# Kernel tuning notes

Hardware: AMD Instinct MI355X
Metric: run time of the kernel (lower is better)

## Reference

```python
import jax, jax.numpy as jnp
import numpy as np

D_MODEL = 768
N_HEADS = 12
D_FF = 3072
EPS = 1e-5


def _layernorm(x, g, b):
    mu = jnp.mean(x, axis=-1, keepdims=True)
    var = jnp.mean(jnp.square(x - mu), axis=-1, keepdims=True)
    return (x - mu) * jax.lax.rsqrt(var + EPS) * g + b


def setup_inputs() -> dict:
    key = jax.random.key(0)
    ks = jax.random.split(key, 16)
    d, f = D_MODEL, D_FF
    s = 1.0 / np.sqrt(d)
    inp = {
        "x": jax.random.normal(ks[0], (1, 4096, d), dtype=jnp.float32),
        "Wq": jax.random.normal(ks[1], (d, d), dtype=jnp.float32) * s,
        "bq": jnp.zeros((d,), jnp.float32),
        "Wk": jax.random.normal(ks[2], (d, d), dtype=jnp.float32) * s,
        "bk": jnp.zeros((d,), jnp.float32),
        "Wv": jax.random.normal(ks[3], (d, d), dtype=jnp.float32) * s,
        "bv": jnp.zeros((d,), jnp.float32),
        "Wo": jax.random.normal(ks[4], (d, d), dtype=jnp.float32) * s,
        "bo": jnp.zeros((d,), jnp.float32),
        "ln1_g": jnp.ones((d,), jnp.float32),
        "ln1_b": jnp.zeros((d,), jnp.float32),
        "ln2_g": jnp.ones((d,), jnp.float32),
        "ln2_b": jnp.zeros((d,), jnp.float32),
        "W1": jax.random.normal(ks[5], (d, f), dtype=jnp.float32) * s,
        "b1": jnp.zeros((f,), jnp.float32),
        "W2": jax.random.normal(ks[6], (f, d), dtype=jnp.float32) * (1.0 / np.sqrt(f)),
        "b2": jnp.zeros((d,), jnp.float32),
    }
    return inp


def reference(x, Wq, bq, Wk, bk, Wv, bv, Wo, bo, ln1_g, ln1_b, ln2_g, ln2_b, W1, b1, W2, b2):
    b, s, d = x.shape
    h = N_HEADS
    dk = d // h

    # --- attention sublayer (pre-norm residual) ---
    xn = _layernorm(x, ln1_g, ln1_b)

    def proj(W, bias):
        y = xn @ W + bias                      # [b, s, d]
        return y.reshape(b, s, h, dk).transpose(0, 2, 1, 3)  # [b, h, s, dk]

    q, k, v = proj(Wq, bq), proj(Wk, bk), proj(Wv, bv)
    scores = jnp.einsum("bhqd,bhkd->bhqk", q, k) / np.sqrt(dk)
    attn = jax.nn.softmax(scores, axis=-1)
    ctx = jnp.einsum("bhqk,bhkd->bhqd", attn, v)
    ctx = ctx.transpose(0, 2, 1, 3).reshape(b, s, d)
    x = x + (ctx @ Wo + bo)

    # --- FFN sublayer (pre-norm residual) ---
    xn2 = _layernorm(x, ln2_g, ln2_b)
    ff = jax.nn.gelu(xn2 @ W1 + b1, approximate=False) @ W2 + b2
    return x + ff
```

## Files before the change

kernel.cpp:

```cpp
#include <hip/hip_runtime.h>
#include <hip/hip_bf16.h>

typedef __attribute__((ext_vector_type(8))) __bf16 bf16x8;
typedef __attribute__((ext_vector_type(4))) __bf16 bf16x4;
typedef __attribute__((ext_vector_type(4))) float f32x4;
typedef __attribute__((ext_vector_type(4))) unsigned short u16x4;
typedef unsigned short ushort_t;

__device__ __forceinline__ ushort_t f2bf(float f) {
    union { float f; unsigned u; } v; v.f = f;
    unsigned r = v.u + 0x7fffu + ((v.u >> 16) & 1u);
    return (ushort_t)(r >> 16);
}

__device__ __forceinline__ void gload16(const ushort_t* g, ushort_t* l) {
    __builtin_amdgcn_global_load_lds(
        (const __attribute__((address_space(1))) unsigned int*)g,
        (__attribute__((address_space(3))) unsigned int*)l,
        16, 0, 0);
}

__device__ __forceinline__ void ln_row(const float* __restrict__ xr,
                                       const float* __restrict__ g,
                                       const float* __restrict__ b,
                                       ushort_t* __restrict__ orow, int t) {
    float v0 = xr[t], v1 = xr[t + 256], v2 = xr[t + 512];
    float s  = v0 + v1 + v2;
    float s2 = v0 * v0 + v1 * v1 + v2 * v2;
#pragma unroll
    for (int off = 32; off; off >>= 1) {
        s  += __shfl_down(s, off);
        s2 += __shfl_down(s2, off);
    }
    __shared__ float red[8];
    const int wid = t >> 6, lane = t & 63;
    if (lane == 0) { red[wid] = s; red[4 + wid] = s2; }
    __syncthreads();
    __shared__ float stats[2];
    if (t == 0) {
        float S = red[0] + red[1] + red[2] + red[3];
        float S2 = red[4] + red[5] + red[6] + red[7];
        float mu = S * (1.0f / 768.0f);
        float var = S2 * (1.0f / 768.0f) - mu * mu;
        stats[0] = mu;
        stats[1] = rsqrtf(var + 1e-5f);
    }
    __syncthreads();
    const float mu = stats[0], rs = stats[1];
    orow[t]       = f2bf((v0 - mu) * rs * g[t]       + b[t]);
    orow[t + 256] = f2bf((v1 - mu) * rs * g[t + 256] + b[t + 256]);
    orow[t + 512] = f2bf((v2 - mu) * rs * g[t + 512] + b[t + 512]);
}

__global__ __launch_bounds__(256) void ln_kernel(const float* __restrict__ x,
                                                 const float* __restrict__ g,
                                                 const float* __restrict__ b,
                                                 ushort_t* __restrict__ out) {
    const int row = blockIdx.x;
    ln_row(x + (size_t)row * 768, g, b, out + (size_t)row * 768, threadIdx.x);
}

__global__ __launch_bounds__(256) void prep_ln(
    const float* __restrict__ Wq, const float* __restrict__ Wk,
    const float* __restrict__ Wv, const float* __restrict__ Wo,
    const float* __restrict__ W1, const float* __restrict__ W2,
    const float* __restrict__ bq, const float* __restrict__ bk,
    const float* __restrict__ bv,
    const float* __restrict__ x, const float* __restrict__ ln1_g,
    const float* __restrict__ ln1_b,
    ushort_t* __restrict__ WqkvT, ushort_t* __restrict__ WoT,
    ushort_t* __restrict__ W1T, ushort_t* __restrict__ W2T,
    float* __restrict__ bqkv, ushort_t* __restrict__ xn) {
    const int bid = blockIdx.x;
    const int t = threadIdx.x;
    if (bid >= 6915) {
        const int row = bid - 6915;
        ln_row(x + (size_t)row * 768, ln1_g, ln1_b, xn + (size_t)row * 768, t);
        return;
    }
    if (bid >= 6912) {
        const int i = bid - 6912;
        const float* s = (i == 0) ? bq : (i == 1) ? bk : bv;
#pragma unroll
        for (int j = t; j < 768; j += 256) bqkv[i * 768 + j] = s[j];
        return;
    }
    const float* src; ushort_t* dst; int R, C, ti;
    if (bid < 576)       { src = Wq; dst = WqkvT;               R = 768;  C = 768;  ti = bid; }
    else if (bid < 1152) { src = Wk; dst = WqkvT + 768 * 768;   R = 768;  C = 768;  ti = bid - 576; }
    else if (bid < 1728) { src = Wv; dst = WqkvT + 2 * 768 * 768; R = 768; C = 768; ti = bid - 1152; }
    else if (bid < 2304) { src = Wo; dst = WoT;                 R = 768;  C = 768;  ti = bid - 1728; }
    else if (bid < 4608) { src = W1; dst = W1T;                 R = 768;  C = 3072; ti = bid - 2304; }
    else                 { src = W2; dst = W2T;                 R = 3072; C = 768;  ti = bid - 4608; }
    const int tpr = C >> 5;
    const int c0 = (ti % tpr) * 32, r0 = (ti / tpr) * 32;
    __shared__ float tile[32][33];
    {
        const int c = t & 31, r = t >> 5;
#pragma unroll
        for (int i = 0; i < 4; i++)
            tile[r + i * 8][c] = src[(size_t)(r0 + r + i * 8) * C + c0 + c];
    }
    __syncthreads();
    {
        const int oc = t >> 3, q = t & 7;
        u16x4 o;
#pragma unroll
        for (int k = 0; k < 4; k++) o[k] = f2bf(tile[q * 4 + k][oc]);
        *(u16x4*)&dst[(size_t)(c0 + oc) * R + r0 + q * 4] = o;
    }
}

template <int BN, int GELU, int RES, int OUTF, int OUTB, int OUTV>
__global__ __launch_bounds__(256, 3)
void gemm_bt(const ushort_t* __restrict__ A, const ushort_t* __restrict__ Bt,
             const float* __restrict__ bias, const float* __restrict__ res,
             float* __restrict__ outF, ushort_t* __restrict__ outB, int ldo,
             ushort_t* __restrict__ outV,
             int M, int N, int K) {
    constexpr int TR  = 128 + BN;
    constexpr int LL  = TR / 64;
    constexpr int WCF = BN / 32;
    __shared__ __align__(16) ushort_t Ls[2][TR * 32];

    const int nbx = gridDim.x;
    const int nwg = nbx * gridDim.y;
    int fb = blockIdx.y * nbx + blockIdx.x;
    fb = (fb & 7) * (nwg >> 3) + (fb >> 3);
    const int m0 = (fb / nbx) * 128, n0 = (fb % nbx) * BN;

    const int t = threadIdx.x;
    const int wid = t >> 6, lane = t & 63;
    const int wr = wid >> 1, wc = wid & 1;
    const int row16 = lane & 15, kg = lane >> 4;
    const int kb = kg * 8;

    const int srow = lane >> 2, scol = (lane & 3) * 8;
    const ushort_t* gsrc[LL];
    int lofs[LL];
#pragma unroll
    for (int i = 0; i < LL; i++) {
        const int r0 = wid * (TR / 4) + 16 * i;
        gsrc[i] = (r0 < 128 ? A + (size_t)(m0 + r0 + srow) * K
                            : Bt + (size_t)(n0 + r0 - 128 + srow) * K) + scol;
        lofs[i] = r0 * 32;
    }

#define STAGE(buf, kofs) do {                                        \
        _Pragma("unroll")                                            \
        for (int i = 0; i < LL; i++)                                 \
            gload16(gsrc[i] + (kofs), &Ls[buf][lofs[i]]);            \
    } while (0)

    f32x4 acc[4][WCF] = {};
    const int NS = K >> 5;
    STAGE(0, 0);
    STAGE(1, 32);
    int cur = 0;

    for (int s = 0; s < NS; ++s) {
        if (s + 1 == NS) asm volatile("s_waitcnt vmcnt(0)" ::: "memory");
        else             asm volatile("s_waitcnt vmcnt(%0)" :: "i"(LL) : "memory");
        __builtin_amdgcn_s_barrier();

        bf16x8 a[4], b[WCF];
#pragma unroll
        for (int i = 0; i < 4; i++)
            a[i] = *(const bf16x8*)&Ls[cur][(wr * 64 + i * 16 + row16) * 32 + kb];
#pragma unroll
        for (int j = 0; j < WCF; j++)
            b[j] = *(const bf16x8*)&Ls[cur][(128 + wc * (BN / 2) + j * 16 + row16) * 32 + kb];
        asm volatile("s_waitcnt lgkmcnt(0)" ::: "memory");
        __builtin_amdgcn_s_barrier();
        if (s + 2 < NS) STAGE(cur, (s + 2) * 32);

        __builtin_amdgcn_s_setprio(1);
#pragma unroll
        for (int i = 0; i < 4; i++)
#pragma unroll
            for (int j = 0; j < WCF; j++)
                acc[i][j] = __builtin_amdgcn_mfma_f32_16x16x32_bf16(a[i], b[j], acc[i][j], 0, 0, 0);
        __builtin_amdgcn_s_setprio(0);
        cur ^= 1;
    }
#undef STAGE

#pragma unroll
    for (int i = 0; i < 4; i++)
#pragma unroll
        for (int j = 0; j < WCF; j++) {
            const int col = n0 + wc * (BN / 2) + j * 16 + row16;
            const float bv = bias[col];
            const int rb = m0 + wr * 64 + i * 16 + kg * 4;
            if (OUTV && col >= 1536) {
                bf16x4 pk;
#pragma unroll
                for (int r = 0; r < 4; r++) pk[r] = (__bf16)(acc[i][j][r] + bv);
                *(bf16x4*)&outV[(size_t)(col - 1536) * 4096 + rb] = pk;
            } else {
#pragma unroll
                for (int r = 0; r < 4; r++) {
                    const int row = rb + r;
                    float v = acc[i][j][r] + bv;
                    if (GELU) {
                        float u = v + 0.044715f * v * v * v;
                        float e = __builtin_amdgcn_exp2f(2.30220779f * u);
                        v = v * e * __builtin_amdgcn_rcpf(e + 1.0f);
                    }
                    if (RES) v += res[(size_t)row * N + col];
                    if (OUTF) outF[(size_t)row * N + col] = v;
                    if (OUTB) outB[(size_t)row * ldo + col] = f2bf(v);
                }
            }
        }
}

__device__ __forceinline__ int swz(int row, int col) {
    return row * 64 + (col ^ ((row & 7) << 3));
}

__global__ __launch_bounds__(256, 3)
void attn_kernel(const ushort_t* __restrict__ qk,
                 const ushort_t* __restrict__ Vt,
                 float* __restrict__ num0, float* __restrict__ num1,
                 float* __restrict__ den) {
    int fb = blockIdx.y * 32 + blockIdx.x;
    fb = (fb & 7) * 96 + (fb >> 3);
    const int q0 = (fb & 31) * 128;
    const int hs = fb >> 5;
    const int h = hs >> 1, sp = hs & 1;
    const int kt0 = sp * 32;

    const int t  = threadIdx.x;
    const int w = t >> 6, lane = t & 63;
    const int row16 = lane & 15, kg = lane >> 4;
    const int kb = kg * 8;

    __shared__ __align__(16) ushort_t Ps[128 * 64];
    __shared__ __align__(16) ushort_t Ks[2][64 * 64];
    __shared__ __align__(16) ushort_t Vs[2][64 * 64];

    {
        const int qr = t >> 1, cb = (t & 1) * 32;
        const size_t qbase = (size_t)(q0 + qr) * 1536 + h * 64 + cb;
#pragma unroll
        for (int j = 0; j < 4; j++)
            *(uint4*)&Ps[swz(qr, cb + j * 8)] = *(const uint4*)&qk[qbase + j * 8];
    }
    {
        const int sr = t >> 2, sc = (t & 3) * 8;
        const size_t kbase = (size_t)(kt0 * 64 + sr) * 1536 + 768 + h * 64 + sc;
        *(uint4*)&Ks[0][swz(sr, sc)]      = *(const uint4*)&qk[kbase];
        *(uint4*)&Ks[0][swz(sr, sc + 32)] = *(const uint4*)&qk[kbase + 32];
        const size_t vbase = (size_t)(h * 64 + sr) * 4096 + kt0 * 64 + sc;
        *(uint4*)&Vs[0][swz(sr, sc)]      = *(const uint4*)&Vt[vbase];
        *(uint4*)&Vs[0][swz(sr, sc + 32)] = *(const uint4*)&Vt[vbase + 32];
    }
    bf16x8 qa0[2], qa1[2];
#pragma unroll
    for (int qb = 0; qb < 2; qb++) {
        qa0[qb] = *(const bf16x8*)&Ps[swz(w * 32 + qb * 16 + row16, kb)];
        qa1[qb] = *(const bf16x8*)&Ps[swz(w * 32 + qb * 16 + row16, 32 + kb)];
    }
    __syncthreads();

    const int rr = lane >> 3;
    const int gcol = ((lane & 7) ^ rr) * 8;
    const ushort_t* gK = qk + 768 + h * 64 + gcol + (size_t)(w * 16 + rr) * 1536;
    const ushort_t* gV = Vt + (size_t)(h * 64 + w * 16 + rr) * 4096 + gcol;

    bf16x8 vones;
#pragma unroll
    for (int i = 0; i < 8; i++) vones[i] = (__bf16)1.0f;

    f32x4 o_acc[2][4] = {};
    f32x4 o_l[2] = {};
    int cur = 0;
    const float SC = 0.18033688011112042f;

    for (int it = 0; it < 32; ++it) {
        if (it != 31) {
            const int kv1 = (kt0 + it + 1) * 64;
            ushort_t* kd = &Ks[cur ^ 1][w * 1024];
            ushort_t* vd = &Vs[cur ^ 1][w * 1024];
            gload16(gK + (size_t)kv1 * 1536,       kd);
            gload16(gK + (size_t)(kv1 + 8) * 1536, kd + 512);
            gload16(gV + kv1,                      vd);
            gload16(gV + kv1 + 8 * 4096,           vd + 512);
        }

        const ushort_t* Kc = Ks[cur];
        const ushort_t* Vc = Vs[cur];

        bf16x8 ka0[4], ka1[4];
#pragma unroll
        for (int f = 0; f < 4; f++) {
            ka0[f] = *(const bf16x8*)&Kc[swz(f * 16 + row16, kb)];
            ka1[f] = *(const bf16x8*)&Kc[swz(f * 16 + row16, 32 + kb)];
        }

        f32x4 s_acc[2][4];
        __builtin_amdgcn_s_setprio(1);
#pragma unroll
        for (int qb = 0; qb < 2; qb++)
#pragma unroll
            for (int f = 0; f < 4; f++) {
                f32x4 z = {};
                z = __builtin_amdgcn_mfma_f32_16x16x32_bf16(ka0[f], qa0[qb], z, 0, 0, 0);
                s_acc[qb][f] = __builtin_amdgcn_mfma_f32_16x16x32_bf16(ka1[f], qa1[qb], z, 0, 0, 0);
            }
        __builtin_amdgcn_s_setprio(0);

#pragma unroll
        for (int qb = 0; qb < 2; qb++)
#pragma unroll
            for (int f = 0; f < 4; f++) {
                bf16x4 pk;
#pragma unroll
                for (int r = 0; r < 4; r++)
                    pk[r] = (__bf16)__builtin_amdgcn_exp2f(fminf(s_acc[qb][f][r] * SC, 30.0f));
                *(bf16x4*)&Ps[swz(w * 32 + qb * 16 + row16, f * 16 + kg * 4)] = pk;
            }

        bf16x8 pa0[2], pa1[2];
#pragma unroll
        for (int qb = 0; qb < 2; qb++) {
            pa0[qb] = *(const bf16x8*)&Ps[swz(w * 32 + qb * 16 + row16, kb)];
            pa1[qb] = *(const bf16x8*)&Ps[swz(w * 32 + qb * 16 + row16, 32 + kb)];
        }
        __builtin_amdgcn_s_setprio(1);
#pragma unroll
        for (int f = 0; f < 4; f++) {
            bf16x8 vb0 = *(const bf16x8*)&Vc[swz(f * 16 + row16, kb)];
            bf16x8 vb1 = *(const bf16x8*)&Vc[swz(f * 16 + row16, 32 + kb)];
#pragma unroll
            for (int qb = 0; qb < 2; qb++) {
                o_acc[qb][f] = __builtin_amdgcn_mfma_f32_16x16x32_bf16(pa0[qb], vb0, o_acc[qb][f], 0, 0, 0);
                o_acc[qb][f] = __builtin_amdgcn_mfma_f32_16x16x32_bf16(pa1[qb], vb1, o_acc[qb][f], 0, 0, 0);
            }
        }
#pragma unroll
        for (int qb = 0; qb < 2; qb++) {
            o_l[qb] = __builtin_amdgcn_mfma_f32_16x16x32_bf16(pa0[qb], vones, o_l[qb], 0, 0, 0);
            o_l[qb] = __builtin_amdgcn_mfma_f32_16x16x32_bf16(pa1[qb], vones, o_l[qb], 0, 0, 0);
        }
        __builtin_amdgcn_s_setprio(0);

        __syncthreads();
        cur ^= 1;
    }

    float* np = sp ? num1 : num0;
#pragma unroll
    for (int qb = 0; qb < 2; qb++)
#pragma unroll
        for (int f = 0; f < 4; f++)
#pragma unroll
            for (int r = 0; r < 4; r++) {
                const int qrow = q0 + w * 32 + qb * 16 + kg * 4 + r;
                np[(size_t)qrow * 768 + h * 64 + f * 16 + row16] = o_acc[qb][f][r];
            }
    if (row16 == 0 && h == 0) {
    }
    if (row16 == 0) {
#pragma unroll
        for (int qb = 0; qb < 2; qb++)
#pragma unroll
            for (int r = 0; r < 4; r++) {
                const int qrow = q0 + w * 32 + qb * 16 + kg * 4 + r;
                den[((size_t)sp * 12 + h) * 4096 + qrow] = o_l[qb][r];
            }
    }
}

__global__ __launch_bounds__(256) void attn_combine(
    const float* __restrict__ num0, const float* __restrict__ num1,
    const float* __restrict__ den, ushort_t* __restrict__ ctx) {
    const int idx = blockIdx.x * 256 + threadIdx.x;
    const int q = idx / 192;
    const int g = idx % 192;
    const int h = g >> 4;
    const float rd = __builtin_amdgcn_rcpf(den[(size_t)h * 4096 + q] +
                                           den[((size_t)12 + h) * 4096 + q]);
    const size_t o = (size_t)q * 768 + g * 4;
    float4 a = *(const float4*)&num0[o];
    float4 b = *(const float4*)&num1[o];
    u16x4 pk;
    pk[0] = f2bf((a.x + b.x) * rd);
    pk[1] = f2bf((a.y + b.y) * rd);
    pk[2] = f2bf((a.z + b.z) * rd);
    pk[3] = f2bf((a.w + b.w) * rd);
    *(u16x4*)&ctx[o] = pk;
}

extern "C" void kernel_launch(void* const* d_in, const int* in_sizes, int n_in,
                              void* d_out, int out_size, void* d_ws, size_t ws_size,
                              hipStream_t stream) {
    const float* x     = (const float*)d_in[0];
    const float* Wq    = (const float*)d_in[1];
    const float* bq    = (const float*)d_in[2];
    const float* Wk    = (const float*)d_in[3];
    const float* bk    = (const float*)d_in[4];
    const float* Wv    = (const float*)d_in[5];
    const float* bv    = (const float*)d_in[6];
    const float* Wo    = (const float*)d_in[7];
    const float* bo    = (const float*)d_in[8];
    const float* ln1_g = (const float*)d_in[9];
    const float* ln1_b = (const float*)d_in[10];
    const float* ln2_g = (const float*)d_in[11];
    const float* ln2_b = (const float*)d_in[12];
    const float* W1    = (const float*)d_in[13];
    const float* b1    = (const float*)d_in[14];
    const float* W2    = (const float*)d_in[15];
    const float* b2    = (const float*)d_in[16];

    char* ws = (char*)d_ws;
    ushort_t* WqkvT = (ushort_t*)ws; ws += (size_t)2304 * 768 * 2;
    ushort_t* WoT   = (ushort_t*)ws; ws += (size_t)768 * 768 * 2;
    ushort_t* W1T   = (ushort_t*)ws; ws += (size_t)3072 * 768 * 2;
    ushort_t* W2T   = (ushort_t*)ws; ws += (size_t)768 * 3072 * 2;
    float*    bqkv  = (float*)ws;    ws += (size_t)2304 * 4;
    ushort_t* xn    = (ushort_t*)ws; ws += (size_t)4096 * 768 * 2;
    ushort_t* qk    = (ushort_t*)ws; ws += (size_t)4096 * 1536 * 2;
    ushort_t* Vtb   = (ushort_t*)ws; ws += (size_t)768 * 4096 * 2;
    ushort_t* ctxb  = (ushort_t*)ws; ws += (size_t)4096 * 768 * 2;
    float*    x1    = (float*)ws;    ws += (size_t)4096 * 768 * 4;
    float*    num1  = (float*)ws;    ws += (size_t)4096 * 768 * 4;
    float*    den   = (float*)ws;    ws += (size_t)2 * 12 * 4096 * 4;
    ushort_t* H     = qk;
    float*    num0  = x1;

    prep_ln<<<6915 + 4096, 256, 0, stream>>>(Wq, Wk, Wv, Wo, W1, W2, bq, bk, bv,
                                             x, ln1_g, ln1_b,
                                             WqkvT, WoT, W1T, W2T, bqkv, xn);

    gemm_bt<128, 0, 0, 0, 1, 1><<<dim3(18, 32), 256, 0, stream>>>(
        xn, WqkvT, bqkv, nullptr, nullptr, qk, 1536, Vtb, 4096, 2304, 768);

    attn_kernel<<<dim3(32, 24), 256, 0, stream>>>(qk, Vtb, num0, num1, den);
    attn_combine<<<3072, 256, 0, stream>>>(num0, num1, den, ctxb);

    gemm_bt<64, 0, 1, 1, 0, 0><<<dim3(12, 32), 256, 0, stream>>>(
        ctxb, WoT, bo, x, x1, nullptr, 0, nullptr, 4096, 768, 768);

    ln_kernel<<<4096, 256, 0, stream>>>(x1, ln2_g, ln2_b, xn);
    gemm_bt<128, 1, 0, 0, 1, 0><<<dim3(24, 32), 256, 0, stream>>>(
        xn, W1T, b1, nullptr, nullptr, H, 3072, nullptr, 4096, 3072, 768);
    gemm_bt<64, 0, 1, 1, 0, 0><<<dim3(12, 32), 256, 0, stream>>>(
        H, W2T, b2, x1, (float*)d_out, nullptr, 0, nullptr, 4096, 768, 3072);

    (void)in_sizes; (void)n_in; (void)out_size; (void)ws_size;
}
```

Measured before the change: 201.3 us.

## Rewrite attention inner loop with 32x32 MFMA and register-resident P fragments

Switches the attention QK^T and PV products from 16x16x32 to 32x32x16 bf16 MFMA, computing S transposed so each lane holds a column of probabilities. The exponentiated P is packed to bf16 and moved into the PV operand layout in registers with cvt_pk and permlane32_swap, so the LDS round trip through Ps is gone. The softmax denominator becomes a scalar per-lane sum instead of extra MFMAs against a ones vector. This cuts LDS traffic and MFMA count per tile, but raises register pressure from 16-wide accumulators and relies on gfx950-specific instructions.

Result: no change. 205.2 us (+1.9%).

```diff
diff --git a/kernel.cpp b/kernel.cpp
--- a/kernel.cpp
+++ b/kernel.cpp
@@ -4,6 +4,7 @@
 typedef __attribute__((ext_vector_type(8))) __bf16 bf16x8;
 typedef __attribute__((ext_vector_type(4))) __bf16 bf16x4;
 typedef __attribute__((ext_vector_type(4))) float f32x4;
+typedef __attribute__((ext_vector_type(16))) float f32x16;
 typedef __attribute__((ext_vector_type(4))) unsigned short u16x4;
 typedef unsigned short ushort_t;
 
@@ -219,6 +220,19 @@
     return row * 64 + (col ^ ((row & 7) << 3));
 }
 
+#define PFRAG(parr, base, frag) do {                                               \
+    unsigned U0, U1, W0, W1;                                                       \
+    asm("v_cvt_pk_bf16_f32 %0, %1, %2" : "=v"(U0) : "v"(parr[base+0]), "v"(parr[base+1])); \
+    asm("v_cvt_pk_bf16_f32 %0, %1, %2" : "=v"(U1) : "v"(parr[base+2]), "v"(parr[base+3])); \
+    asm("v_cvt_pk_bf16_f32 %0, %1, %2" : "=v"(W0) : "v"(parr[base+4]), "v"(parr[base+5])); \
+    asm("v_cvt_pk_bf16_f32 %0, %1, %2" : "=v"(W1) : "v"(parr[base+6]), "v"(parr[base+7])); \
+    asm("v_permlane32_swap_b32 %0, %1" : "+v"(U0), "+v"(W0));                      \
+    asm("v_permlane32_swap_b32 %0, %1" : "+v"(U1), "+v"(W1));                      \
+    union { unsigned u[4]; bf16x8 v; } pk_;                                        \
+    pk_.u[0] = U0; pk_.u[1] = U1; pk_.u[2] = W0; pk_.u[3] = W1;                    \
+    frag = pk_.v;                                                                  \
+} while (0)
+
 __global__ __launch_bounds__(256, 3)
 void attn_kernel(const ushort_t* __restrict__ qk,
                  const ushort_t* __restrict__ Vt,
@@ -231,12 +245,13 @@
     const int h = hs >> 1, sp = hs & 1;
     const int kt0 = sp * 32;
 
-    const int t  = threadIdx.x;
+    const int t = threadIdx.x;
     const int w = t >> 6, lane = t & 63;
-    const int row16 = lane & 15, kg = lane >> 4;
-    const int kb = kg * 8;
-
-    __shared__ __align__(16) ushort_t Ps[128 * 64];
+    const int l31 = lane & 31;
+    const int hi = lane >> 5;
+    const int hi8 = hi * 8;
+
+    __shared__ __align__(16) ushort_t Qs[128 * 64];
     __shared__ __align__(16) ushort_t Ks[2][64 * 64];
     __shared__ __align__(16) ushort_t Vs[2][64 * 64];
 
@@ -245,7 +260,7 @@
         const size_t qbase = (size_t)(q0 + qr) * 1536 + h * 64 + cb;
 #pragma unroll
         for (int j = 0; j < 4; j++)
-            *(uint4*)&Ps[swz(qr, cb + j * 8)] = *(const uint4*)&qk[qbase + j * 8];
+            *(uint4*)&Qs[swz(qr, cb + j * 8)] = *(const uint4*)&qk[qbase + j * 8];
     }
     {
         const int sr = t >> 2, sc = (t & 3) * 8;
@@ -256,25 +271,20 @@
         *(uint4*)&Vs[0][swz(sr, sc)]      = *(const uint4*)&Vt[vbase];
         *(uint4*)&Vs[0][swz(sr, sc + 32)] = *(const uint4*)&Vt[vbase + 32];
     }
-    bf16x8 qa0[2], qa1[2];
-#pragma unroll
-    for (int qb = 0; qb < 2; qb++) {
-        qa0[qb] = *(const bf16x8*)&Ps[swz(w * 32 + qb * 16 + row16, kb)];
-        qa1[qb] = *(const bf16x8*)&Ps[swz(w * 32 + qb * 16 + row16, 32 + kb)];
-    }
     __syncthreads();
+
+    const bf16x8 qf0 = *(const bf16x8*)&Qs[swz(w * 32 + l31, hi8)];
+    const bf16x8 qf1 = *(const bf16x8*)&Qs[swz(w * 32 + l31, 16 + hi8)];
+    const bf16x8 qf2 = *(const bf16x8*)&Qs[swz(w * 32 + l31, 32 + hi8)];
+    const bf16x8 qf3 = *(const bf16x8*)&Qs[swz(w * 32 + l31, 48 + hi8)];
 
     const int rr = lane >> 3;
     const int gcol = ((lane & 7) ^ rr) * 8;
     const ushort_t* gK = qk + 768 + h * 64 + gcol + (size_t)(w * 16 + rr) * 1536;
     const ushort_t* gV = Vt + (size_t)(h * 64 + w * 16 + rr) * 4096 + gcol;
 
-    bf16x8 vones;
-#pragma unroll
-    for (int i = 0; i < 8; i++) vones[i] = (__bf16)1.0f;
-
-    f32x4 o_acc[2][4] = {};
-    f32x4 o_l[2] = {};
+    f32x16 oA = {}, oB = {};
+    float o_den = 0.0f;
     int cur = 0;
     const float SC = 0.18033688011112042f;
 
@@ -292,85 +302,77 @@
         const ushort_t* Kc = Ks[cur];
         const ushort_t* Vc = Vs[cur];
 
-        bf16x8 ka0[4], ka1[4];
-#pragma unroll
-        for (int f = 0; f < 4; f++) {
-            ka0[f] = *(const bf16x8*)&Kc[swz(f * 16 + row16, kb)];
-            ka1[f] = *(const bf16x8*)&Kc[swz(f * 16 + row16, 32 + kb)];
-        }
-
-        f32x4 s_acc[2][4];
+        f32x16 s0 = {}, s1 = {};
         __builtin_amdgcn_s_setprio(1);
-#pragma unroll
-        for (int qb = 0; qb < 2; qb++)
-#pragma unroll
-            for (int f = 0; f < 4; f++) {
-                f32x4 z = {};
-                z = __builtin_amdgcn_mfma_f32_16x16x32_bf16(ka0[f], qa0[qb], z, 0, 0, 0);
-                s_acc[qb][f] = __builtin_amdgcn_mfma_f32_16x16x32_bf16(ka1[f], qa1[qb], z, 0, 0, 0);
-            }
-        __builtin_amdgcn_s_setprio(0);
-
-#pragma unroll
-        for (int qb = 0; qb < 2; qb++)
-#pragma unroll
-            for (int f = 0; f < 4; f++) {
-                bf16x4 pk;
-#pragma unroll
-                for (int r = 0; r < 4; r++)
-                    pk[r] = (__bf16)__builtin_amdgcn_exp2f(fminf(s_acc[qb][f][r] * SC, 30.0f));
-                *(bf16x4*)&Ps[swz(w * 32 + qb * 16 + row16, f * 16 + kg * 4)] = pk;
-            }
-
-        bf16x8 pa0[2], pa1[2];
-#pragma unroll
-        for (int qb = 0; qb < 2; qb++) {
-            pa0[qb] = *(const bf16x8*)&Ps[swz(w * 32 + qb * 16 + row16, kb)];
-            pa1[qb] = *(const bf16x8*)&Ps[swz(w * 32 + qb * 16 + row16, 32 + kb)];
-        }
-        __builtin_amdgcn_s_setprio(1);
-#pragma unroll
-        for (int f = 0; f < 4; f++) {
-            bf16x8 vb0 = *(const bf16x8*)&Vc[swz(f * 16 + row16, kb)];
-            bf16x8 vb1 = *(const bf16x8*)&Vc[swz(f * 16 + row16, 32 + kb)];
-#pragma unroll
-            for (int qb = 0; qb < 2; qb++) {
-                o_acc[qb][f] = __builtin_amdgcn_mfma_f32_16x16x32_bf16(pa0[qb], vb0, o_acc[qb][f], 0, 0, 0);
-                o_acc[qb][f] = __builtin_amdgcn_mfma_f32_16x16x32_bf16(pa1[qb], vb1, o_acc[qb][f], 0, 0, 0);
-            }
-        }
-#pragma unroll
-        for (int qb = 0; qb < 2; qb++) {
-            o_l[qb] = __builtin_amdgcn_mfma_f32_16x16x32_bf16(pa0[qb], vones, o_l[qb], 0, 0, 0);
-            o_l[qb] = __builtin_amdgcn_mfma_f32_16x16x32_bf16(pa1[qb], vones, o_l[qb], 0, 0, 0);
+        {
+            bf16x8 k0, k1;
+            k0 = *(const bf16x8*)&Kc[swz(l31, hi8)];
+            k1 = *(const bf16x8*)&Kc[swz(32 + l31, hi8)];
+            s0 = __builtin_amdgcn_mfma_f32_32x32x16_bf16(k0, qf0, s0, 0, 0, 0);
+            s1 = __builtin_amdgcn_mfma_f32_32x32x16_bf16(k1, qf0, s1, 0, 0, 0);
+            k0 = *(const bf16x8*)&Kc[swz(l31, 16 + hi8)];
+            k1 = *(const bf16x8*)&Kc[swz(32 + l31, 16 + hi8)];
+            s0 = __builtin_amdgcn_mfma_f32_32x32x16_bf16(k0, qf1, s0, 0, 0, 0);
+            s1 = __builtin_amdgcn_mfma_f32_32x32x16_bf16(k1, qf1, s1, 0, 0, 0);
+            k0 = *(const bf16x8*)&Kc[swz(l31, 32 + hi8)];
+            k1 = *(const bf16x8*)&Kc[swz(32 + l31, 32 + hi8)];
+            s0 = __builtin_amdgcn_mfma_f32_32x32x16_bf16(k0, qf2, s0, 0, 0, 0);
+            s1 = __builtin_amdgcn_mfma_f32_32x32x16_bf16(k1, qf2, s1, 0, 0, 0);
+            k0 = *(const bf16x8*)&Kc[swz(l31, 48 + hi8)];
+            k1 = *(const bf16x8*)&Kc[swz(32 + l31, 48 + hi8)];
+            s0 = __builtin_amdgcn_mfma_f32_32x32x16_bf16(k0, qf3, s0, 0, 0, 0);
+            s1 = __builtin_amdgcn_mfma_f32_32x32x16_bf16(k1, qf3, s1, 0, 0, 0);
         }
         __builtin_amdgcn_s_setprio(0);
 
+        float p0[16], p1[16];
+#pragma unroll
+        for (int r = 0; r < 16; r++) {
+            p0[r] = __builtin_amdgcn_exp2f(fminf(s0[r] * SC, 30.0f));
+            p1[r] = __builtin_amdgcn_exp2f(fminf(s1[r] * SC, 30.0f));
+            o_den += p0[r] + p1[r];
+        }
+
+        bf16x8 pf, vA, vB;
+        __builtin_amdgcn_s_setprio(1);
+        PFRAG(p0, 0, pf);
+        vA = *(const bf16x8*)&Vc[swz(l31, hi8)];
+        vB = *(const bf16x8*)&Vc[swz(32 + l31, hi8)];
+        oA = __builtin_amdgcn_mfma_f32_32x32x16_bf16(vA, pf, oA, 0, 0, 0);
+        oB = __builtin_amdgcn_mfma_f32_32x32x16_bf16(vB, pf, oB, 0, 0, 0);
+        PFRAG(p0, 8, pf);
+        vA = *(const bf16x8*)&Vc[swz(l31, 16 + hi8)];
+        vB = *(const bf16x8*)&Vc[swz(32 + l31, 16 + hi8)];
+        oA = __builtin_amdgcn_mfma_f32_32x32x16_bf16(vA, pf, oA, 0, 0, 0);
+        oB = __builtin_amdgcn_mfma_f32_32x32x16_bf16(vB, pf, oB, 0, 0, 0);
+        PFRAG(p1, 0, pf);
+        vA = *(const bf16x8*)&Vc[swz(l31, 32 + hi8)];
+        vB = *(const bf16x8*)&Vc[swz(32 + l31, 32 + hi8)];
+        oA = __builtin_amdgcn_mfma_f32_32x32x16_bf16(vA, pf, oA, 0, 0, 0);
+        oB = __builtin_amdgcn_mfma_f32_32x32x16_bf16(vB, pf, oB, 0, 0, 0);
+        PFRAG(p1, 8, pf);
+        vA = *(const bf16x8*)&Vc[swz(l31, 48 + hi8)];
+        vB = *(const bf16x8*)&Vc[swz(32 + l31, 48 + hi8)];
+        oA = __builtin_amdgcn_mfma_f32_32x32x16_bf16(vA, pf, oA, 0, 0, 0);
+        oB = __builtin_amdgcn_mfma_f32_32x32x16_bf16(vB, pf, oB, 0, 0, 0);
+        __builtin_amdgcn_s_setprio(0);
+
         __syncthreads();
         cur ^= 1;
     }
 
+    o_den += __shfl_xor(o_den, 32);
     float* np = sp ? num1 : num0;
-#pragma unroll
-    for (int qb = 0; qb < 2; qb++)
-#pragma unroll
-        for (int f = 0; f < 4; f++)
-#pragma unroll
-            for (int r = 0; r < 4; r++) {
-                const int qrow = q0 + w * 32 + qb * 16 + kg * 4 + r;
-                np[(size_t)qrow * 768 + h * 64 + f * 16 + row16] = o_acc[qb][f][r];
-            }
-    if (row16 == 0 && h == 0) {
-    }
-    if (row16 == 0) {
-#pragma unroll
-        for (int qb = 0; qb < 2; qb++)
-#pragma unroll
-            for (int r = 0; r < 4; r++) {
-                const int qrow = q0 + w * 32 + qb * 16 + kg * 4 + r;
-                den[((size_t)sp * 12 + h) * 4096 + qrow] = o_l[qb][r];
-            }
-    }
+    const int qrow = q0 + w * 32 + l31;
+    float* orow = np + (size_t)qrow * 768 + h * 64 + hi * 4;
+#pragma unroll
+    for (int qd = 0; qd < 4; qd++) {
+        f32x4 a = { oA[4 * qd], oA[4 * qd + 1], oA[4 * qd + 2], oA[4 * qd + 3] };
+        *(f32x4*)&orow[qd * 8] = a;
+        f32x4 b = { oB[4 * qd], oB[4 * qd + 1], oB[4 * qd + 2], oB[4 * qd + 3] };
+        *(f32x4*)&orow[32 + qd * 8] = b;
+    }
+    if (hi == 0) den[((size_t)sp * 12 + h) * 4096 + qrow] = o_den;
 }
 
 __global__ __launch_bounds__(256) void attn_combine(
```

## Split-K the Wo and W2 GEMMs and fuse Wo reduction with LN2

Applied to the files above, without the earlier changes.

Replaces the Wo and W2 projections with a split-K GEMM that launches two K halves as separate blocks writing fp32 partials, doubling the grid from 384 to 768 workgroups for better CU occupancy on these narrow N=768 outputs. The Wo partials are summed with bias and residual inside a new fused LN2 kernel, replacing the separate layernorm kernel. The W2 partials are combined by a small elementwise kernel. This adds extra fp32 partial traffic and one more launch for W2.

After: 204.3 us. Within noise of the previous version (+1.5%).

```diff
diff --git a/kernel.cpp b/kernel.cpp
--- a/kernel.cpp
+++ b/kernel.cpp
@@ -50,14 +50,6 @@
     orow[t]       = f2bf((v0 - mu) * rs * g[t]       + b[t]);
     orow[t + 256] = f2bf((v1 - mu) * rs * g[t + 256] + b[t + 256]);
     orow[t + 512] = f2bf((v2 - mu) * rs * g[t + 512] + b[t + 512]);
-}
-
-__global__ __launch_bounds__(256) void ln_kernel(const float* __restrict__ x,
-                                                 const float* __restrict__ g,
-                                                 const float* __restrict__ b,
-                                                 ushort_t* __restrict__ out) {
-    const int row = blockIdx.x;
-    ln_row(x + (size_t)row * 768, g, b, out + (size_t)row * 768, threadIdx.x);
 }
 
 __global__ __launch_bounds__(256) void prep_ln(
@@ -215,6 +207,151 @@
         }
 }
 
+__global__ __launch_bounds__(256, 3)
+void gemm_part(const ushort_t* __restrict__ A, const ushort_t* __restrict__ Bt,
+               float* __restrict__ p0, float* __restrict__ p1,
+               int M, int N, int K, int Klen) {
+    constexpr int TR = 192, BK = 64, LL = 6;
+    __shared__ __align__(16) ushort_t Ls[2][TR * BK];
+
+    const int nbx = gridDim.x;
+    const int nwg = nbx * gridDim.y;
+    int fb = blockIdx.y * nbx + blockIdx.x;
+    fb = (fb & 7) * (nwg >> 3) + (fb >> 3);
+    const int m0 = (fb / nbx) * 128, n0 = (fb % nbx) * 64;
+    const int kOff = blockIdx.z * Klen;
+    float* outP = blockIdx.z ? p1 : p0;
+
+    const int t = threadIdx.x;
+    const int wid = t >> 6, lane = t & 63;
+    const int wr = wid >> 1, wc = wid & 1;
+    const int row16 = lane & 15, kg = lane >> 4;
+    const int rsw = row16 & 7;
+
+    const int srow = lane >> 3;
+    const int sslot = (lane & 7) ^ srow;
+    const ushort_t* gsrc[LL];
+    int lofs[LL];
+#pragma unroll
+    for (int i = 0; i < LL; i++) {
+        const int r0 = wid * 48 + 8 * i;
+        gsrc[i] = (r0 < 128 ? A + (size_t)(m0 + r0 + srow) * K
+                            : Bt + (size_t)(n0 + r0 - 128 + srow) * K) + kOff + sslot * 8;
+        lofs[i] = r0 * BK;
+    }
+
+#define STAGEP(buf, kofs) do {                                       \
+        _Pragma("unroll")                                            \
+        for (int i = 0; i < LL; i++)                                 \
+            gload16(gsrc[i] + (kofs), &Ls[buf][lofs[i]]);            \
+    } while (0)
+
+    f32x4 acc[4][2] = {};
+    const int NS = Klen >> 6;
+    STAGEP(0, 0);
+    STAGEP(1, BK);
+    int cur = 0;
+
+    for (int s = 0; s < NS; ++s) {
+        if (s + 1 == NS) asm volatile("s_waitcnt vmcnt(0)" ::: "memory");
+        else             asm volatile("s_waitcnt vmcnt(%0)" :: "i"(LL) : "memory");
+        __builtin_amdgcn_s_barrier();
+
+        bf16x8 a[2][4], b[2][2];
+#pragma unroll
+        for (int kk = 0; kk < 2; kk++) {
+            const int sA = ((kk * 4 + kg) ^ rsw) * 8;
+#pragma unroll
+            for (int i = 0; i < 4; i++)
+                a[kk][i] = *(const bf16x8*)&Ls[cur][(wr * 64 + i * 16 + row16) * BK + sA];
+#pragma unroll
+            for (int j = 0; j < 2; j++)
+                b[kk][j] = *(const bf16x8*)&Ls[cur][(128 + wc * 32 + j * 16 + row16) * BK + sA];
+        }
+        asm volatile("s_waitcnt lgkmcnt(0)" ::: "memory");
+        __builtin_amdgcn_s_barrier();
+        if (s + 2 < NS) STAGEP(cur, (s + 2) * BK);
+
+        __builtin_amdgcn_s_setprio(1);
+#pragma unroll
+        for (int kk = 0; kk < 2; kk++)
+#pragma unroll
+            for (int i = 0; i < 4; i++)
+#pragma unroll
+                for (int j = 0; j < 2; j++)
+                    acc[i][j] = __builtin_amdgcn_mfma_f32_16x16x32_bf16(a[kk][i], b[kk][j], acc[i][j], 0, 0, 0);
+        __builtin_amdgcn_s_setprio(0);
+        cur ^= 1;
+    }
+#undef STAGEP
+
+#pragma unroll
+    for (int i = 0; i < 4; i++)
+#pragma unroll
+        for (int j = 0; j < 2; j++) {
+            const int col = n0 + wc * 32 + j * 16 + row16;
+            const int rb = m0 + wr * 64 + i * 16 + kg * 4;
+#pragma unroll
+            for (int r = 0; r < 4; r++)
+                outP[(size_t)(rb + r) * N + col] = acc[i][j][r];
+        }
+}
+
+__global__ __launch_bounds__(256) void ln2wo_kernel(
+    const float* __restrict__ p0, const float* __restrict__ p1,
+    const float* __restrict__ bo, const float* __restrict__ x,
+    const float* __restrict__ g, const float* __restrict__ b,
+    float* __restrict__ x1, ushort_t* __restrict__ xn) {
+    const int row = blockIdx.x, t = threadIdx.x;
+    const size_t base = (size_t)row * 768;
+    float v0 = p0[base + t]       + p1[base + t]       + bo[t]       + x[base + t];
+    float v1 = p0[base + t + 256] + p1[base + t + 256] + bo[t + 256] + x[base + t + 256];
+    float v2 = p0[base + t + 512] + p1[base + t + 512] + bo[t + 512] + x[base + t + 512];
+    x1[base + t] = v0; x1[base + t + 256] = v1; x1[base + t + 512] = v2;
+
+    float s  = v0 + v1 + v2;
+    float s2 = v0 * v0 + v1 * v1 + v2 * v2;
+#pragma unroll
+    for (int off = 32; off; off >>= 1) {
+        s  += __shfl_down(s, off);
+        s2 += __shfl_down(s2, off);
+    }
+    __shared__ float red[8];
+    const int wid = t >> 6, lane = t & 63;
+    if (lane == 0) { red[wid] = s; red[4 + wid] = s2; }
+    __syncthreads();
+    __shared__ float stats[2];
+    if (t == 0) {
+        float S = red[0] + red[1] + red[2] + red[3];
+        float S2 = red[4] + red[5] + red[6] + red[7];
+        float mu = S * (1.0f / 768.0f);
+        float var = S2 * (1.0f / 768.0f) - mu * mu;
+        stats[0] = mu;
+        stats[1] = rsqrtf(var + 1e-5f);
+    }
+    __syncthreads();
+    const float mu = stats[0], rs = stats[1];
+    ushort_t* orow = xn + base;
+    orow[t]       = f2bf((v0 - mu) * rs * g[t]       + b[t]);
+    orow[t + 256] = f2bf((v1 - mu) * rs * g[t + 256] + b[t + 256]);
+    orow[t + 512] = f2bf((v2 - mu) * rs * g[t + 512] + b[t + 512]);
+}
+
+__global__ __launch_bounds__(256) void w2comb_kernel(
+    const float* __restrict__ p0, const float* __restrict__ p1,
+    const float* __restrict__ b2, const float* __restrict__ x1,
+    float* __restrict__ out) {
+    const size_t o = ((size_t)blockIdx.x * 256 + threadIdx.x) * 4;
+    const int col = (int)(o % 768);
+    float4 a = *(const float4*)&p0[o];
+    float4 b = *(const float4*)&p1[o];
+    float4 r = *(const float4*)&x1[o];
+    float4 bb = *(const float4*)&b2[col];
+    float4 v = { a.x + b.x + r.x + bb.x, a.y + b.y + r.y + bb.y,
+                 a.z + b.z + r.z + bb.z, a.w + b.w + r.w + bb.w };
+    *(float4*)&out[o] = v;
+}
+
 __device__ __forceinline__ int swz(int row, int col) {
     return row * 64 + (col ^ ((row & 7) << 3));
 }
@@ -360,8 +497,6 @@
                 const int qrow = q0 + w * 32 + qb * 16 + kg * 4 + r;
                 np[(size_t)qrow * 768 + h * 64 + f * 16 + row16] = o_acc[qb][f][r];
             }
-    if (row16 == 0 && h == 0) {
-    }
     if (row16 == 0) {
 #pragma unroll
         for (int qb = 0; qb < 2; qb++)
@@ -427,8 +562,10 @@
     float*    x1    = (float*)ws;    ws += (size_t)4096 * 768 * 4;
     float*    num1  = (float*)ws;    ws += (size_t)4096 * 768 * 4;
     float*    den   = (float*)ws;    ws += (size_t)2 * 12 * 4096 * 4;
+    float*    pB    = (float*)ws;    ws += (size_t)4096 * 768 * 4;
     ushort_t* H     = qk;
     float*    num0  = x1;
+    float*    pA    = num1;
 
     prep_ln<<<6915 + 4096, 256, 0, stream>>>(Wq, Wk, Wv, Wo, W1, W2, bq, bk, bv,
                                              x, ln1_g, ln1_b,
@@ -440,14 +577,15 @@
     attn_kernel<<<dim3(32, 24), 256, 0, stream>>>(qk, Vtb, num0, num1, den);
     attn_combine<<<3072, 256, 0, stream>>>(num0, num1, den, ctxb);
 
-    gemm_bt<64, 0, 1, 1, 0, 0><<<dim3(12, 32), 256, 0, stream>>>(
-        ctxb, WoT, bo, x, x1, nullptr, 0, nullptr, 4096, 768, 768);
-
-    ln_kernel<<<4096, 256, 0, stream>>>(x1, ln2_g, ln2_b, xn);
+    gemm_part<<<dim3(12, 32, 2), 256, 0, stream>>>(ctxb, WoT, pA, pB,
+                                                   4096, 768, 768, 384);
+    ln2wo_kernel<<<4096, 256, 0, stream>>>(pA, pB, bo, x, ln2_g, ln2_b, x1, xn);
+
     gemm_bt<128, 1, 0, 0, 1, 0><<<dim3(24, 32), 256, 0, stream>>>(
         xn, W1T, b1, nullptr, nullptr, H, 3072, nullptr, 4096, 3072, 768);
-    gemm_bt<64, 0, 1, 1, 0, 0><<<dim3(12, 32), 256, 0, stream>>>(
-        H, W2T, b2, x1, (float*)d_out, nullptr, 0, nullptr, 4096, 768, 3072);
+    gemm_part<<<dim3(12, 32, 2), 256, 0, stream>>>(H, W2T, pA, pB,
+                                                   4096, 768, 3072, 1536);
+    w2comb_kernel<<<3072, 256, 0, stream>>>(pA, pB, b2, x1, (float*)d_out);
 
     (void)in_sizes; (void)n_in; (void)out_size; (void)ws_size;
 }
```

## Load attention K/V directly from global to registers and store partials in bf16

Applied to the files above, without the earlier changes.

The attention kernel drops its LDS double-buffered K/V staging and the per-iteration barrier, reading each wave's K and V fragments straight from global memory into registers. The softmax denominator is now summed in registers with cross-lane shuffles, replacing the extra ones-vector MFMAs. The split-KV partial numerators are written as bf16 instead of fp32, halving traffic into the combine kernel, which now processes eight elements per thread. Risks: every wave re-reads K/V from global/L2 with no cross-wave sharing, global load latency is no longer hidden by prefetch, and bf16 partials lose some precision.

Measured after the change: 304.7 us. +51.4%, slower.

```diff
diff --git a/kernel.cpp b/kernel.cpp
--- a/kernel.cpp
+++ b/kernel.cpp
@@ -5,6 +5,7 @@
 typedef __attribute__((ext_vector_type(4))) __bf16 bf16x4;
 typedef __attribute__((ext_vector_type(4))) float f32x4;
 typedef __attribute__((ext_vector_type(4))) unsigned short u16x4;
+typedef __attribute__((ext_vector_type(8))) unsigned short u16x8;
 typedef unsigned short ushort_t;
 
 __device__ __forceinline__ ushort_t f2bf(float f) {
@@ -222,7 +223,7 @@
 __global__ __launch_bounds__(256, 3)
 void attn_kernel(const ushort_t* __restrict__ qk,
                  const ushort_t* __restrict__ Vt,
-                 float* __restrict__ num0, float* __restrict__ num1,
+                 ushort_t* __restrict__ num0, ushort_t* __restrict__ num1,
                  float* __restrict__ den) {
     int fb = blockIdx.y * 32 + blockIdx.x;
     fb = (fb & 7) * 96 + (fb >> 3);
@@ -237,8 +238,6 @@
     const int kb = kg * 8;
 
     __shared__ __align__(16) ushort_t Ps[128 * 64];
-    __shared__ __align__(16) ushort_t Ks[2][64 * 64];
-    __shared__ __align__(16) ushort_t Vs[2][64 * 64];
 
     {
         const int qr = t >> 1, cb = (t & 1) * 32;
@@ -247,56 +246,38 @@
         for (int j = 0; j < 4; j++)
             *(uint4*)&Ps[swz(qr, cb + j * 8)] = *(const uint4*)&qk[qbase + j * 8];
     }
-    {
-        const int sr = t >> 2, sc = (t & 3) * 8;
-        const size_t kbase = (size_t)(kt0 * 64 + sr) * 1536 + 768 + h * 64 + sc;
-        *(uint4*)&Ks[0][swz(sr, sc)]      = *(const uint4*)&qk[kbase];
-        *(uint4*)&Ks[0][swz(sr, sc + 32)] = *(const uint4*)&qk[kbase + 32];
-        const size_t vbase = (size_t)(h * 64 + sr) * 4096 + kt0 * 64 + sc;
-        *(uint4*)&Vs[0][swz(sr, sc)]      = *(const uint4*)&Vt[vbase];
-        *(uint4*)&Vs[0][swz(sr, sc + 32)] = *(const uint4*)&Vt[vbase + 32];
-    }
     bf16x8 qa0[2], qa1[2];
 #pragma unroll
     for (int qb = 0; qb < 2; qb++) {
         qa0[qb] = *(const bf16x8*)&Ps[swz(w * 32 + qb * 16 + row16, kb)];
         qa1[qb] = *(const bf16x8*)&Ps[swz(w * 32 + qb * 16 + row16, 32 + kb)];
     }
-    __syncthreads();
-
-    const int rr = lane >> 3;
-    const int gcol = ((lane & 7) ^ rr) * 8;
-    const ushort_t* gK = qk + 768 + h * 64 + gcol + (size_t)(w * 16 + rr) * 1536;
-    const ushort_t* gV = Vt + (size_t)(h * 64 + w * 16 + rr) * 4096 + gcol;
-
-    bf16x8 vones;
-#pragma unroll
-    for (int i = 0; i < 8; i++) vones[i] = (__bf16)1.0f;
+
+    const ushort_t* gKf[4];
+    const ushort_t* gVf[4];
+#pragma unroll
+    for (int f = 0; f < 4; f++) {
+        gKf[f] = qk + (size_t)(kt0 * 64 + f * 16 + row16) * 1536 + 768 + h * 64 + kb;
+        gVf[f] = Vt + (size_t)(h * 64 + f * 16 + row16) * 4096 + kt0 * 64 + kb;
+    }
 
     f32x4 o_acc[2][4] = {};
-    f32x4 o_l[2] = {};
-    int cur = 0;
+    float den_r[2] = {0.0f, 0.0f};
     const float SC = 0.18033688011112042f;
 
     for (int it = 0; it < 32; ++it) {
-        if (it != 31) {
-            const int kv1 = (kt0 + it + 1) * 64;
-            ushort_t* kd = &Ks[cur ^ 1][w * 1024];
-            ushort_t* vd = &Vs[cur ^ 1][w * 1024];
-            gload16(gK + (size_t)kv1 * 1536,       kd);
-            gload16(gK + (size_t)(kv1 + 8) * 1536, kd + 512);
-            gload16(gV + kv1,                      vd);
-            gload16(gV + kv1 + 8 * 4096,           vd + 512);
+        bf16x8 ka0[4], ka1[4], vb0[4], vb1[4];
+        const size_t kofs = (size_t)it * (64 * 1536);
+        const int vofs = it * 64;
+#pragma unroll
+        for (int f = 0; f < 4; f++) {
+            ka0[f] = *(const bf16x8*)(gKf[f] + kofs);
+            ka1[f] = *(const bf16x8*)(gKf[f] + kofs + 32);
         }
-
-        const ushort_t* Kc = Ks[cur];
-        const ushort_t* Vc = Vs[cur];
-
-        bf16x8 ka0[4], ka1[4];
 #pragma unroll
         for (int f = 0; f < 4; f++) {
-            ka0[f] = *(const bf16x8*)&Kc[swz(f * 16 + row16, kb)];
-            ka1[f] = *(const bf16x8*)&Kc[swz(f * 16 + row16, 32 + kb)];
+            vb0[f] = *(const bf16x8*)(gVf[f] + vofs);
+            vb1[f] = *(const bf16x8*)(gVf[f] + vofs + 32);
         }
 
         f32x4 s_acc[2][4];
@@ -317,8 +298,11 @@
             for (int f = 0; f < 4; f++) {
                 bf16x4 pk;
 #pragma unroll
-                for (int r = 0; r < 4; r++)
-                    pk[r] = (__bf16)__builtin_amdgcn_exp2f(fminf(s_acc[qb][f][r] * SC, 30.0f));
+                for (int r = 0; r < 4; r++) {
+                    float pv = __builtin_amdgcn_exp2f(fminf(s_acc[qb][f][r] * SC, 30.0f));
+                    den_r[qb] += pv;
+                    pk[r] = (__bf16)pv;
+                }
                 *(bf16x4*)&Ps[swz(w * 32 + qb * 16 + row16, f * 16 + kg * 4)] = pk;
             }
 
@@ -330,27 +314,22 @@
         }
         __builtin_amdgcn_s_setprio(1);
 #pragma unroll
-        for (int f = 0; f < 4; f++) {
-            bf16x8 vb0 = *(const bf16x8*)&Vc[swz(f * 16 + row16, kb)];
-            bf16x8 vb1 = *(const bf16x8*)&Vc[swz(f * 16 + row16, 32 + kb)];
+        for (int f = 0; f < 4; f++)
 #pragma unroll
             for (int qb = 0; qb < 2; qb++) {
-                o_acc[qb][f] = __builtin_amdgcn_mfma_f32_16x16x32_bf16(pa0[qb], vb0, o_acc[qb][f], 0, 0, 0);
-                o_acc[qb][f] = __builtin_amdgcn_mfma_f32_16x16x32_bf16(pa1[qb], vb1, o_acc[qb][f], 0, 0, 0);
+                o_acc[qb][f] = __builtin_amdgcn_mfma_f32_16x16x32_bf16(pa0[qb], vb0[f], o_acc[qb][f], 0, 0, 0);
+                o_acc[qb][f] = __builtin_amdgcn_mfma_f32_16x16x32_bf16(pa1[qb], vb1[f], o_acc[qb][f], 0, 0, 0);
             }
-        }
-#pragma unroll
-        for (int qb = 0; qb < 2; qb++) {
-            o_l[qb] = __builtin_amdgcn_mfma_f32_16x16x32_bf16(pa0[qb], vones, o_l[qb], 0, 0, 0);
-            o_l[qb] = __builtin_amdgcn_mfma_f32_16x16x32_bf16(pa1[qb], vones, o_l[qb], 0, 0, 0);
-        }
         __builtin_amdgcn_s_setprio(0);
-
-        __syncthreads();
-        cur ^= 1;
-    }
-
-    float* np = sp ? num1 : num0;
+    }
+
+#pragma unroll
+    for (int qb = 0; qb < 2; qb++) {
+        den_r[qb] += __shfl_xor(den_r[qb], 16);
+        den_r[qb] += __shfl_xor(den_r[qb], 32);
+    }
+
+    ushort_t* np = sp ? num1 : num0;
 #pragma unroll
     for (int qb = 0; qb < 2; qb++)
 #pragma unroll
@@ -358,39 +337,37 @@
 #pragma unroll
             for (int r = 0; r < 4; r++) {
                 const int qrow = q0 + w * 32 + qb * 16 + kg * 4 + r;
-                np[(size_t)qrow * 768 + h * 64 + f * 16 + row16] = o_acc[qb][f][r];
+                np[(size_t)qrow * 768 + h * 64 + f * 16 + row16] = f2bf(o_acc[qb][f][r]);
             }
-    if (row16 == 0 && h == 0) {
-    }
-    if (row16 == 0) {
-#pragma unroll
-        for (int qb = 0; qb < 2; qb++)
-#pragma unroll
-            for (int r = 0; r < 4; r++) {
-                const int qrow = q0 + w * 32 + qb * 16 + kg * 4 + r;
-                den[((size_t)sp * 12 + h) * 4096 + qrow] = o_l[qb][r];
-            }
+    if (kg == 0) {
+#pragma unroll
+        for (int qb = 0; qb < 2; qb++) {
+            const int qrow = q0 + w * 32 + qb * 16 + row16;
+            den[((size_t)sp * 12 + h) * 4096 + qrow] = den_r[qb];
+        }
     }
 }
 
 __global__ __launch_bounds__(256) void attn_combine(
-    const float* __restrict__ num0, const float* __restrict__ num1,
+    const ushort_t* __restrict__ num0, const ushort_t* __restrict__ num1,
     const float* __restrict__ den, ushort_t* __restrict__ ctx) {
     const int idx = blockIdx.x * 256 + threadIdx.x;
-    const int q = idx / 192;
-    const int g = idx % 192;
-    const int h = g >> 4;
+    const int q = idx / 96;
+    const int g = idx % 96;
+    const int h = g >> 3;
     const float rd = __builtin_amdgcn_rcpf(den[(size_t)h * 4096 + q] +
                                            den[((size_t)12 + h) * 4096 + q]);
-    const size_t o = (size_t)q * 768 + g * 4;
-    float4 a = *(const float4*)&num0[o];
-    float4 b = *(const float4*)&num1[o];
-    u16x4 pk;
-    pk[0] = f2bf((a.x + b.x) * rd);
-    pk[1] = f2bf((a.y + b.y) * rd);
-    pk[2] = f2bf((a.z + b.z) * rd);
-    pk[3] = f2bf((a.w + b.w) * rd);
-    *(u16x4*)&ctx[o] = pk;
+    const size_t o = (size_t)q * 768 + g * 8;
+    u16x8 a = *(const u16x8*)&num0[o];
+    u16x8 b = *(const u16x8*)&num1[o];
+    u16x8 pk;
+#pragma unroll
+    for (int i = 0; i < 8; i++) {
+        const float av = __uint_as_float((unsigned)a[i] << 16);
+        const float bv = __uint_as_float((unsigned)b[i] << 16);
+        pk[i] = f2bf((av + bv) * rd);
+    }
+    *(u16x8*)&ctx[o] = pk;
 }
 
 extern "C" void kernel_launch(void* const* d_in, const int* in_sizes, int n_in,
@@ -425,10 +402,10 @@
     ushort_t* Vtb   = (ushort_t*)ws; ws += (size_t)768 * 4096 * 2;
     ushort_t* ctxb  = (ushort_t*)ws; ws += (size_t)4096 * 768 * 2;
     float*    x1    = (float*)ws;    ws += (size_t)4096 * 768 * 4;
-    float*    num1  = (float*)ws;    ws += (size_t)4096 * 768 * 4;
+    ushort_t* num0b = (ushort_t*)ws; ws += (size_t)4096 * 768 * 2;
+    ushort_t* num1b = (ushort_t*)ws; ws += (size_t)4096 * 768 * 2;
     float*    den   = (float*)ws;    ws += (size_t)2 * 12 * 4096 * 4;
     ushort_t* H     = qk;
-    float*    num0  = x1;
 
     prep_ln<<<6915 + 4096, 256, 0, stream>>>(Wq, Wk, Wv, Wo, W1, W2, bq, bk, bv,
                                              x, ln1_g, ln1_b,
@@ -437,8 +414,8 @@
     gemm_bt<128, 0, 0, 0, 1, 1><<<dim3(18, 32), 256, 0, stream>>>(
         xn, WqkvT, bqkv, nullptr, nullptr, qk, 1536, Vtb, 4096, 2304, 768);
 
-    attn_kernel<<<dim3(32, 24), 256, 0, stream>>>(qk, Vtb, num0, num1, den);
-    attn_combine<<<3072, 256, 0, stream>>>(num0, num1, den, ctxb);
+    attn_kernel<<<dim3(32, 24), 256, 0, stream>>>(qk, Vtb, num0b, num1b, den);
+    attn_combine<<<1536, 256, 0, stream>>>(num0b, num1b, den, ctxb);
 
     gemm_bt<64, 0, 1, 1, 0, 0><<<dim3(12, 32), 256, 0, stream>>>(
         ctxb, WoT, bo, x, x1, nullptr, 0, nullptr, 4096, 768, 768);
```
